# Kernel tuning notes

Measured on AMD Instinct MI355X. Metric: run time of the kernel, lower is better.

The kernel has to match this reference:

```python
import jax, jax.numpy as jnp
import numpy as np
from functools import partial

ALPHA = 0.5
BETA = 0.5
THRESHOLD = 0.5


def _ccl(fg):
    """Connected-component labeling (4-connectivity) of a 2D bool mask via
    iterative min-label propagation; background = 0, components get distinct
    positive ids (component-wise min of raster index + 1). Matches the
    component partition of scipy.ndimage.label (ids differ, masks identical)."""
    H, W = fg.shape
    BIG = H * W + 2
    init = jnp.where(fg, jnp.arange(1, H * W + 1, dtype=jnp.int32).reshape(H, W), 0)

    def step(lab):
        l = jnp.where(fg, lab, BIG)
        up = jnp.pad(l, ((1, 0), (0, 0)), constant_values=BIG)[:-1]
        dn = jnp.pad(l, ((0, 1), (0, 0)), constant_values=BIG)[1:]
        lf = jnp.pad(l, ((0, 0), (1, 0)), constant_values=BIG)[:, :-1]
        rt = jnp.pad(l, ((0, 0), (0, 1)), constant_values=BIG)[:, 1:]
        m = jnp.minimum(jnp.minimum(jnp.minimum(up, dn), jnp.minimum(lf, rt)), l)
        return jnp.where(fg, m, 0)

    def cond(c):
        return jnp.any(c[0] != c[1])

    def body(c):
        return (step(c[0]), c[0])

    lab, _ = jax.lax.while_loop(cond, body, (step(init), init))
    return lab


def _critical(a_lab, b_lab, n_seg):
    """Binary mask of components of a_lab that are not fully covered by the
    foreground of b_lab (i.e. contain at least one mistake voxel) -- the
    detect_critical split/merge criterion."""
    miss = ((b_lab == 0) & (a_lab > 0)).astype(jnp.int32)
    counts = jax.ops.segment_sum(miss.ravel(), a_lab.ravel(), num_segments=n_seg)
    return jnp.where(a_lab > 0, (counts[a_lab] > 0).astype(jnp.float32), 0.0)


def _critical_masks(preds, targets):
    # preds/targets: [B,1,H,W]; work on channel-0 2D slices as the module does
    p2 = preds[:, 0]
    t2 = targets[:, 0]
    H, W = p2.shape[-2:]
    n_seg = H * W + 1
    plab = jax.vmap(_ccl)(p2 > THRESHOLD)
    tlab = jax.vmap(_ccl)(t2 > 0)
    crit = jax.vmap(partial(_critical, n_seg=n_seg))
    neg = crit(tlab, plab)   # critical_type = -1: target components missed
    pos = crit(plab, tlab)   # critical_type = +1: pred components wrong
    return BETA * neg + (1.0 - BETA) * pos  # [B,H,W]


def setup_inputs() -> dict:
    key = jax.random.key(0)
    k1, k2 = jax.random.split(key)
    preds = jax.random.normal(k1, (16, 1, 1024, 1024), dtype=jnp.float32)
    targets = (jax.random.uniform(k2, (16, 1, 1024, 1024)) > 0.5).astype(jnp.float32)
    return {"preds": preds, "targets": targets}


def reference(preds, targets):
    # BCEWithLogitsLoss(reduction='none'), numerically stable
    loss = jnp.maximum(preds, 0) - preds * targets + jnp.log1p(jnp.exp(-jnp.abs(preds)))
    mask = _critical_masks(preds, targets)  # [B,H,W], constant wrt grads
    weight = (1.0 - ALPHA) + ALPHA * mask[:, None]  # broadcast over channel dim
    return (weight * loss).mean()
```

## Files before the change

### kernel.cpp

```cpp
#include <hip/hip_runtime.h>
#include <math.h>


#define HH 1024
#define WW 1024
#define IMGPIX (HH * WW)
#define NB_TOTAL 16
#define FLAGBIT 0x40000000
#define IDXMASK 0x3FFFFFFF
#define NBLK 2048
#define NPART 2048
#define NTHR 256
#define WPR 16
#define RPR 512
#define SROWS 32
#define STRIPS (HH / SROWS)
#define SLOTS (SROWS * RPR)
#define NTHR_S 1024

typedef unsigned long long u64;

__device__ __forceinline__ int findRootH(int* p, int i) {
    volatile int* vp = p;
    int r = i;
    int e = vp[r] & IDXMASK;
    while (e != r) {
        int e2 = vp[e] & IDXMASK;
        if (e2 != e) p[r] = e2;
        r = e; e = e2;
    }
    return r;
}

__device__ __forceinline__ void flagProp(int* p, int x) {
    while (true) {
        int r = findRootH(p, x);
        int old = atomicOr(&p[r], FLAGBIT);
        if ((old & IDXMASK) == r) return;
        x = old & IDXMASK;
    }
}

__device__ __forceinline__ void uniteGF(int* p, int a, int b) {
    int ra = findRootH(p, a), rb = findRootH(p, b);
    while (ra != rb) {
        if (ra < rb) { int t = ra; ra = rb; rb = t; }
        int e = p[ra];
        if ((e & IDXMASK) != ra) { ra = findRootH(p, e & IDXMASK); continue; }
        int prev = atomicCAS(&p[ra], e, rb);
        if (prev == e) {
            if (e & FLAGBIT) flagProp(p, rb);
            return;
        }
        ra = findRootH(p, prev & IDXMASK);
        rb = findRootH(p, rb);
    }
}

__device__ __forceinline__ int findRootL(int* lab, int i) {
    volatile int* vl = lab;
    int r = i;
    int e = vl[r] & IDXMASK;
    while (e != r) {
        int e2 = vl[e] & IDXMASK;
        if (e2 != e) lab[r] = e2;
        r = e; e = e2;
    }
    return r;
}

__device__ __forceinline__ void uniteL(int* lab, int a, int b) {
    int ra = findRootL(lab, a), rb = findRootL(lab, b);
    while (ra != rb) {
        if (ra < rb) { int t = ra; ra = rb; rb = t; }
        int prev = atomicCAS(&lab[ra], ra, rb);
        if (prev == ra) return;
        ra = findRootL(lab, prev & IDXMASK);
        rb = findRootL(lab, rb);
    }
}

__device__ __forceinline__ int runIndexW(u64 starts, int b) {
    u64 below = (2ULL << b) - 1ULL;
    return (int)__popcll(starts & below) - 1;
}

__global__ void k_zero(double* __restrict__ part) {
    part[blockIdx.x * blockDim.x + threadIdx.x] = 0.0;
}

__device__ __forceinline__ float packf(float mag, bool fl) {
    return __uint_as_float(__float_as_uint(mag) | (fl ? 0x80000000u : 0u));
}

__device__ __forceinline__ void phaseBody(int lane, int mask, int mist, int starts,
                                          int carry, int excl, int incl,
                                          const float* lossv, long rbase,
                                          float* __restrict__ runsum) {
    float cur = 0.0f, headmag = 0.0f;
    bool curf = false, headf = false;
    bool begun = false, prevfg = (carry != 0), hasHead = false;
    int scount = 0;
    #pragma unroll
    for (int k = 0; k < 16; ++k) {
        bool fg = (mask >> k) & 1;
        bool mk = (mist >> k) & 1;
        if (fg) {
            if ((starts >> k) & 1) { cur = lossv[k]; curf = mk; begun = true; ++scount; }
            else { cur += lossv[k]; curf |= mk; }
        } else {
            if (prevfg) {
                if (begun) runsum[rbase + excl + scount - 1] = packf(cur, curf);
                else { hasHead = true; headmag = cur; headf = curf; }
            }
        }
        prevfg = fg;
    }
    float sv = prevfg ? packf(cur, curf) : 0.0f;
    u64 fullb = __ballot(mask == 0xFFFF);
    if (fullb) {
        int fl = (starts != 0);
        #pragma unroll
        for (int d = 1; d < 64; d <<= 1) {
            float u = __shfl_up(sv, d, 64);
            int uf = __shfl_up(fl, d, 64);
            if (lane >= d) {
                if (!fl) {
                    unsigned sg = (__float_as_uint(sv) | __float_as_uint(u)) & 0x80000000u;
                    float mag = fabsf(sv) + fabsf(u);
                    sv = __uint_as_float(__float_as_uint(mag) | sg);
                }
                fl |= uf;
            }
        }
    }
    float svprev = __shfl_up(sv, 1, 64);
    if (hasHead) {
        unsigned sg = (__float_as_uint(svprev) & 0x80000000u) | (headf ? 0x80000000u : 0u);
        float mag = fabsf(svprev) + headmag;
        runsum[rbase + excl - 1] = __uint_as_float(__float_as_uint(mag) | sg);
    }
    if (lane == 63 && prevfg) runsum[rbase + incl - 1] = sv;
}

__global__ void k_maskloss(const float* __restrict__ preds, const float* __restrict__ targets,
                           long gbase, int nrows,
                           u64* __restrict__ fT, u64* __restrict__ fP,
                           u64* __restrict__ sT, u64* __restrict__ sP,
                           int* __restrict__ prT, int* __restrict__ prP,
                           int* __restrict__ rcT, int* __restrict__ rcP,
                           float* __restrict__ runsumT, float* __restrict__ runsumP,
                           double* __restrict__ part) {
    __shared__ double sh[4];
    int wid = threadIdx.x >> 6, lane = threadIdx.x & 63;
    double lsum = 0.0;
    for (int R = blockIdx.x * 4 + wid; R < nrows; R += gridDim.x * 4) {
        long pixbase = (long)R * WW;
        long rbase = (long)R * RPR;
        const float4* p4 = (const float4*)(preds + gbase + pixbase);
        const float4* t4 = (const float4*)(targets + gbase + pixbase);
        float lossv[16];
        int maskT = 0, maskP = 0;
        float rowsum = 0.0f;
        #pragma unroll
        for (int j = 0; j < 4; ++j) {
            float4 pv = p4[lane * 4 + j];
            float4 tv = t4[lane * 4 + j];
            float pp[4] = {pv.x, pv.y, pv.z, pv.w};
            float tt[4] = {tv.x, tv.y, tv.z, tv.w};
            #pragma unroll
            for (int q = 0; q < 4; ++q) {
                int k = j * 4 + q;
                float p = pp[q], t = tt[q];
                float loss = fmaxf(p, 0.0f) - p * t + __logf(1.0f + __expf(-fabsf(p)));
                lossv[k] = loss;
                rowsum += loss;
                maskT |= ((int)(t > 0.0f)) << k;
                maskP |= ((int)(p > 0.5f)) << k;
            }
        }
        lsum += (double)rowsum;

        int mistT = maskT & ~maskP;
        int mistP = maskP & ~maskT;

        int pm = __shfl_up(maskT | (maskP << 16), 1, 64);
        int carryT = (lane == 0) ? 0 : ((pm >> 15) & 1);
        int carryP = (lane == 0) ? 0 : ((int)(((unsigned)pm) >> 31) & 1);
        int stT_ = maskT & ~((maskT << 1) | carryT) & 0xFFFF;
        int stP_ = maskP & ~((maskP << 1) | carryP) & 0xFFFF;

        int cntT = __popc(stT_), cntP = __popc(stP_);
        int incl2 = cntT | (cntP << 16);
        #pragma unroll
        for (int d = 1; d < 64; d <<= 1) {
            int u = __shfl_up(incl2, d, 64);
            if (lane >= d) incl2 += u;
        }
        int inclT = incl2 & 0xFFFF;
        int inclP = (int)(((unsigned)incl2) >> 16);
        int exT = inclT - cntT;
        int exP = inclP - cntP;

        phaseBody(lane, maskT, mistT, stT_, carryT, exT, inclT, lossv, rbase, runsumT);
        phaseBody(lane, maskP, mistP, stP_, carryP, exP, inclP, lossv, rbase, runsumP);
        if (lane == 63) { rcT[R] = inclT; rcP[R] = inclP; }

        int subid = lane & 15;
        int srcl = subid * 4;
        u64 fw = 0, sw = 0;
        #pragma unroll
        for (int j = 0; j < 4; ++j) {
            int mT = __shfl(maskT, srcl + j, 64);
            int mP = __shfl(maskP, srcl + j, 64);
            int aT = __shfl(stT_, srcl + j, 64);
            int aP = __shfl(stP_, srcl + j, 64);
            u64 m = (u64)(unsigned)((lane < 16) ? mT : mP);
            u64 a = (u64)(unsigned)((lane < 16) ? aT : aP);
            fw |= (m & 0xFFFFULL) << (16 * j);
            sw |= (a & 0xFFFFULL) << (16 * j);
        }
        int eT = __shfl(exT, srcl, 64);
        int eP = __shfl(exP, srcl, 64);
        int wi = R * WPR + subid;
        if (lane < 16) { fT[wi] = fw; sT[wi] = sw; prT[wi] = eT; }
        else if (lane < 32) { fP[wi] = fw; sP[wi] = sw; prP[wi] = eP; }
    }
    lsum *= 0.5;
    #pragma unroll
    for (int off = 32; off > 0; off >>= 1) lsum += __shfl_down(lsum, off, 64);
    if (lane == 0) sh[wid] = lsum;
    __syncthreads();
    if (threadIdx.x == 0) part[blockIdx.x] += sh[0] + sh[1] + sh[2] + sh[3];
}

__global__ __launch_bounds__(NTHR_S) void
k_strip(const u64* __restrict__ fT, const u64* __restrict__ fP,
        const u64* __restrict__ sT, const u64* __restrict__ sP,
        const int* __restrict__ prT, const int* __restrict__ prP,
        const int* __restrict__ rcT, const int* __restrict__ rcP,
        const float* __restrict__ runsumT, const float* __restrict__ runsumP,
        int* __restrict__ parentT, int* __restrict__ parentP) {
    __shared__ int lab[SLOTS];
    __shared__ int rcL[SROWS];
    int bid = blockIdx.x;
    int ph = bid & 1; bid >>= 1;
    int strip = bid & (STRIPS - 1);
    int img = bid >> 5;
    const u64* f = ph ? fP : fT;
    const u64* s = ph ? sP : sT;
    const int* pr = ph ? prP : prT;
    const int* rc = ph ? rcP : rcT;
    const float* runsum = ph ? runsumP : runsumT;
    int* parent = ph ? parentP : parentT;
    const int row0 = img * HH + strip * SROWS;

    if (threadIdx.x < SROWS) rcL[threadIdx.x] = rc[row0 + threadIdx.x];
    __syncthreads();

    for (int i = threadIdx.x; i < SLOTS; i += NTHR_S)
        if ((i & (RPR - 1)) < rcL[i >> 9]) lab[i] = i;
    __syncthreads();

    for (int task = threadIdx.x; task < (SROWS - 1) * WPR * 2; task += NTHR_S) {
        int j = task & 1, w = (task >> 1) & 15, r = task >> 5;
        int w0 = (row0 + r) * WPR + w, w1 = w0 + WPR;
        u64 o = f[w0] & f[w1];
        if (!o) continue;
        u64 s0 = s[w0], s1 = s[w1];
        int b0 = r * RPR + pr[w0], b1 = (r + 1) * RPR + pr[w1];
        u64 os = o & ~(o << 1);
        int k = 0;
        while (os) {
            int b = __builtin_ctzll(os);
            os &= os - 1;
            if ((k++ & 1) == j)
                uniteL(lab, b0 + runIndexW(s0, b), b1 + runIndexW(s1, b));
        }
    }
    __syncthreads();

    const int gb = row0 * RPR;
    for (int i = threadIdx.x; i < SLOTS; i += NTHR_S) {
        if ((i & (RPR - 1)) >= rcL[i >> 9]) continue;
        int e = lab[i];
        int rt = e & IDXMASK;
        if (rt != i) {
            rt = findRootL(lab, i);
            parent[gb + i] = gb + rt;
        }
        if (__float_as_uint(runsum[gb + i]) >> 31) {
            if (!(((volatile int*)lab)[rt] & FLAGBIT)) atomicOr(&lab[rt], FLAGBIT);
        }
    }
    __syncthreads();

    for (int i = threadIdx.x; i < SLOTS; i += NTHR_S) {
        if ((i & (RPR - 1)) >= rcL[i >> 9]) continue;
        int e = lab[i];
        if ((e & IDXMASK) == i) parent[gb + i] = (gb + i) | (e & FLAGBIT);
    }
}

__global__ void k_bound(const u64* __restrict__ fT, const u64* __restrict__ fP,
                        const u64* __restrict__ sT, const u64* __restrict__ sP,
                        const int* __restrict__ prT, const int* __restrict__ prP,
                        int* __restrict__ parentT, int* __restrict__ parentP, int nb) {
    int tasks = nb * (STRIPS - 1) * WPR * 2;
    int stride = gridDim.x * blockDim.x;
    for (int id = blockIdx.x * blockDim.x + threadIdx.x; id < tasks; id += stride) {
        int ph = id & 1;
        int t = id >> 1;
        int w = t & 15; t >>= 4;
        int bnd = t % (STRIPS - 1);
        int img = t / (STRIPS - 1);
        int R = img * HH + bnd * SROWS + (SROWS - 1);
        const u64* f = ph ? fP : fT;
        const u64* s = ph ? sP : sT;
        const int* pr = ph ? prP : prT;
        int* parent = ph ? parentP : parentT;
        int w0 = R * WPR + w, w1 = w0 + WPR;
        u64 o = f[w0] & f[w1];
        if (!o) continue;
        u64 s0 = s[w0], s1 = s[w1];
        int b0 = R * RPR + pr[w0], b1 = (R + 1) * RPR + pr[w1];
        u64 os = o & ~(o << 1);
        while (os) {
            int b = __builtin_ctzll(os);
            os &= os - 1;
            uniteGF(parent, b0 + runIndexW(s0, b), b1 + runIndexW(s1, b));
        }
    }
}

__global__ void k_accumrun(const int* __restrict__ rcT, const int* __restrict__ rcP,
                           int* __restrict__ parentT, int* __restrict__ parentP,
                           const float* __restrict__ runsumT, const float* __restrict__ runsumP,
                           double* __restrict__ part, int nslots) {
    int stride = gridDim.x * blockDim.x;
    double local = 0.0;
    int ngroups = nslots >> 2;
    for (int g = blockIdx.x * blockDim.x + threadIdx.x; g < ngroups; g += stride) {
        int base = g << 2;
        int row = base >> 9, k = base & (RPR - 1);
        int nT = rcT[row] - k, nP = rcP[row] - k;
        if (nT > 0) {
            int4 e4 = *(const int4*)&parentT[base];
            float4 r4 = *(const float4*)&runsumT[base];
            int ee[4] = {e4.x, e4.y, e4.z, e4.w};
            float rr[4] = {r4.x, r4.y, r4.z, r4.w};
            int n = nT < 4 ? nT : 4;
            for (int j = 0; j < n; ++j) {
                int e = ee[j];
                int r = e & IDXMASK;
                int fl;
                if (r == base + j) fl = e & FLAGBIT;
                else { r = findRootH(parentT, r); fl = parentT[r] & FLAGBIT; }
                if (fl) local += 0.25 * (double)fabsf(rr[j]);
            }
        }
        if (nP > 0) {
            int4 e4 = *(const int4*)&parentP[base];
            float4 r4 = *(const float4*)&runsumP[base];
            int ee[4] = {e4.x, e4.y, e4.z, e4.w};
            float rr[4] = {r4.x, r4.y, r4.z, r4.w};
            int n = nP < 4 ? nP : 4;
            for (int j = 0; j < n; ++j) {
                int e = ee[j];
                int r = e & IDXMASK;
                int fl;
                if (r == base + j) fl = e & FLAGBIT;
                else { r = findRootH(parentP, r); fl = parentP[r] & FLAGBIT; }
                if (fl) local += 0.25 * (double)fabsf(rr[j]);
            }
        }
    }
    #pragma unroll
    for (int off = 32; off > 0; off >>= 1) local += __shfl_down(local, off, 64);
    __shared__ double sh[NTHR / 64];
    int lane = threadIdx.x & 63, wid = threadIdx.x >> 6;
    if (lane == 0) sh[wid] = local;
    __syncthreads();
    if (threadIdx.x == 0) {
        double tot = 0.0;
        #pragma unroll
        for (int w = 0; w < NTHR / 64; ++w) tot += sh[w];
        part[blockIdx.x] += tot;
    }
}

__global__ void k_final(const double* __restrict__ part, float* __restrict__ out, double inv_n) {
    double v = 0.0;
    for (int i = threadIdx.x; i < NPART; i += blockDim.x) v += part[i];
    #pragma unroll
    for (int off = 32; off > 0; off >>= 1) v += __shfl_down(v, off, 64);
    __shared__ double sh[NTHR / 64];
    int lane = threadIdx.x & 63, wid = threadIdx.x >> 6;
    if (lane == 0) sh[wid] = v;
    __syncthreads();
    if (threadIdx.x == 0) {
        double tot = 0.0;
        #pragma unroll
        for (int w = 0; w < NTHR / 64; ++w) tot += sh[w];
        out[0] = (float)(tot * inv_n);
    }
}

extern "C" void kernel_launch(void* const* d_in, const int* in_sizes, int n_in,
                              void* d_out, int out_size, void* d_ws, size_t ws_size,
                              hipStream_t stream) {
    const float* preds = (const float*)d_in[0];
    const float* targets = (const float*)d_in[1];
    float* out = (float*)d_out;

    double* part = (double*)d_ws;
    char* base = (char*)d_ws + NPART * sizeof(double);
    size_t avail = (ws_size > NPART * sizeof(double)) ? ws_size - NPART * sizeof(double) : 0;
    const size_t wpi = (size_t)HH * WPR;
    const size_t runs_pi = (size_t)HH * RPR;
    const size_t per_img = 4 * wpi * sizeof(u64) + 2 * wpi * sizeof(int)
                         + 2 * HH * sizeof(int) + 2 * runs_pi * sizeof(int)
                         + 2 * runs_pi * sizeof(float);
    int chunk = (int)(avail / per_img);
    if (chunk < 1) chunk = 1;
    if (chunk > NB_TOTAL) chunk = NB_TOTAL;

    u64* fT = (u64*)base;
    u64* fP = fT + (size_t)chunk * wpi;
    u64* sT = fP + (size_t)chunk * wpi;
    u64* sP = sT + (size_t)chunk * wpi;
    int* prT = (int*)(sP + (size_t)chunk * wpi);
    int* prP = prT + (size_t)chunk * wpi;
    int* rcT = prP + (size_t)chunk * wpi;
    int* rcP = rcT + (size_t)chunk * HH;
    int* parentT = rcP + (size_t)chunk * HH;
    int* parentP = parentT + (size_t)chunk * runs_pi;
    float* runsumT = (float*)(parentP + (size_t)chunk * runs_pi);
    float* runsumP = runsumT + (size_t)chunk * runs_pi;

    k_zero<<<NPART / NTHR, NTHR, 0, stream>>>(part);

    for (int b0 = 0; b0 < NB_TOTAL; b0 += chunk) {
        int nb = (b0 + chunk <= NB_TOTAL) ? chunk : (NB_TOTAL - b0);
        long gbase = (long)b0 * IMGPIX;
        int nrows = nb * HH;
        int nslots = (int)(nb * runs_pi);

        k_maskloss<<<NBLK, NTHR, 0, stream>>>(preds, targets, gbase, nrows,
                                              fT, fP, sT, sP, prT, prP, rcT, rcP,
                                              runsumT, runsumP, part);
        k_strip<<<nb * STRIPS * 2, NTHR_S, 0, stream>>>(fT, fP, sT, sP, prT, prP,
                                                        rcT, rcP, runsumT, runsumP,
                                                        parentT, parentP);
        k_bound<<<512, NTHR, 0, stream>>>(fT, fP, sT, sP, prT, prP, parentT, parentP, nb);
        k_accumrun<<<NBLK, NTHR, 0, stream>>>(rcT, rcP, parentT, parentP,
                                              runsumT, runsumP, part, nslots);
    }

    double inv_n = 1.0 / ((double)NB_TOTAL * (double)IMGPIX);
    k_final<<<1, NTHR, 0, stream>>>(part, out, inv_n);
}
```

Measured before the change: 242.1 us.

## Fuse mask/loss row pass with per-strip CCL into one kernel

Merges the row-wise mask/loss/run-extraction kernel and the per-strip union-find kernel into one kernel. Each block owns one 32-row strip and handles both target and prediction labelings in sequence, reusing its shared-memory label array. This removes a kernel launch and lets the strip's run data be read back while it is likely still in cache, and the per-row run counts are passed through shared memory. In exchange the grid drops to one 512-thread block per strip instead of a grid-stride loop plus two blocks per strip, and the two phases run serially, which reduces parallelism and occupancy.

Measured after the change: 279.0 us. 15.2% more time.

```diff
diff --git a/kernel.cpp b/kernel.cpp
--- a/kernel.cpp
+++ b/kernel.cpp
@@ -16,7 +16,7 @@
 #define SROWS 32
 #define STRIPS (HH / SROWS)
 #define SLOTS (SROWS * RPR)
-#define NTHR_S 1024
+#define NTHR_F 512
 
 typedef unsigned long long u64;
 
@@ -143,18 +143,30 @@
     if (lane == 63 && prevfg) runsum[rbase + incl - 1] = sv;
 }
 
-__global__ void k_maskloss(const float* __restrict__ preds, const float* __restrict__ targets,
-                           long gbase, int nrows,
-                           u64* __restrict__ fT, u64* __restrict__ fP,
-                           u64* __restrict__ sT, u64* __restrict__ sP,
-                           int* __restrict__ prT, int* __restrict__ prP,
-                           int* __restrict__ rcT, int* __restrict__ rcP,
-                           float* __restrict__ runsumT, float* __restrict__ runsumP,
-                           double* __restrict__ part) {
-    __shared__ double sh[4];
-    int wid = threadIdx.x >> 6, lane = threadIdx.x & 63;
+__global__ __launch_bounds__(NTHR_F) void
+k_mls(const float* __restrict__ preds, const float* __restrict__ targets,
+      long gbase,
+      u64* __restrict__ fT, u64* __restrict__ fP,
+      u64* __restrict__ sT, u64* __restrict__ sP,
+      int* __restrict__ prT, int* __restrict__ prP,
+      int* __restrict__ rcT, int* __restrict__ rcP,
+      float* __restrict__ runsumT, float* __restrict__ runsumP,
+      int* __restrict__ parentT, int* __restrict__ parentP,
+      double* __restrict__ part) {
+    __shared__ int lab[SLOTS];
+    __shared__ int rcL[2][SROWS];
+    __shared__ double shd[NTHR_F / 64];
+
+    const int tid = threadIdx.x;
+    const int wid = tid >> 6, lane = tid & 63;
+    const int img = blockIdx.x >> 5;
+    const int strip = blockIdx.x & (STRIPS - 1);
+    const int row0 = img * HH + strip * SROWS;
+
     double lsum = 0.0;
-    for (int R = blockIdx.x * 4 + wid; R < nrows; R += gridDim.x * 4) {
+    for (int j = 0; j < 4; ++j) {
+        int rl = wid * 4 + j;
+        int R = row0 + rl;
         long pixbase = (long)R * WW;
         long rbase = (long)R * RPR;
         const float4* p4 = (const float4*)(preds + gbase + pixbase);
@@ -163,14 +175,14 @@
         int maskT = 0, maskP = 0;
         float rowsum = 0.0f;
         #pragma unroll
-        for (int j = 0; j < 4; ++j) {
-            float4 pv = p4[lane * 4 + j];
-            float4 tv = t4[lane * 4 + j];
+        for (int jj = 0; jj < 4; ++jj) {
+            float4 pv = p4[lane * 4 + jj];
+            float4 tv = t4[lane * 4 + jj];
             float pp[4] = {pv.x, pv.y, pv.z, pv.w};
             float tt[4] = {tv.x, tv.y, tv.z, tv.w};
             #pragma unroll
             for (int q = 0; q < 4; ++q) {
-                int k = j * 4 + q;
+                int k = jj * 4 + q;
                 float p = pp[q], t = tt[q];
                 float loss = fmaxf(p, 0.0f) - p * t + __logf(1.0f + __expf(-fabsf(p)));
                 lossv[k] = loss;
@@ -204,21 +216,24 @@
 
         phaseBody(lane, maskT, mistT, stT_, carryT, exT, inclT, lossv, rbase, runsumT);
         phaseBody(lane, maskP, mistP, stP_, carryP, exP, inclP, lossv, rbase, runsumP);
-        if (lane == 63) { rcT[R] = inclT; rcP[R] = inclP; }
+        if (lane == 63) {
+            rcT[R] = inclT; rcP[R] = inclP;
+            rcL[0][rl] = inclT; rcL[1][rl] = inclP;
+        }
 
         int subid = lane & 15;
         int srcl = subid * 4;
         u64 fw = 0, sw = 0;
         #pragma unroll
-        for (int j = 0; j < 4; ++j) {
-            int mT = __shfl(maskT, srcl + j, 64);
-            int mP = __shfl(maskP, srcl + j, 64);
-            int aT = __shfl(stT_, srcl + j, 64);
-            int aP = __shfl(stP_, srcl + j, 64);
+        for (int jj = 0; jj < 4; ++jj) {
+            int mT = __shfl(maskT, srcl + jj, 64);
+            int mP = __shfl(maskP, srcl + jj, 64);
+            int aT = __shfl(stT_, srcl + jj, 64);
+            int aP = __shfl(stP_, srcl + jj, 64);
             u64 m = (u64)(unsigned)((lane < 16) ? mT : mP);
             u64 a = (u64)(unsigned)((lane < 16) ? aT : aP);
-            fw |= (m & 0xFFFFULL) << (16 * j);
-            sw |= (a & 0xFFFFULL) << (16 * j);
+            fw |= (m & 0xFFFFULL) << (16 * jj);
+            sw |= (a & 0xFFFFULL) << (16 * jj);
         }
         int eT = __shfl(exT, srcl, 64);
         int eP = __shfl(exP, srcl, 64);
@@ -229,76 +244,65 @@
     lsum *= 0.5;
     #pragma unroll
     for (int off = 32; off > 0; off >>= 1) lsum += __shfl_down(lsum, off, 64);
-    if (lane == 0) sh[wid] = lsum;
+    if (lane == 0) shd[wid] = lsum;
     __syncthreads();
-    if (threadIdx.x == 0) part[blockIdx.x] += sh[0] + sh[1] + sh[2] + sh[3];
-}
-
-__global__ __launch_bounds__(NTHR_S) void
-k_strip(const u64* __restrict__ fT, const u64* __restrict__ fP,
-        const u64* __restrict__ sT, const u64* __restrict__ sP,
-        const int* __restrict__ prT, const int* __restrict__ prP,
-        const int* __restrict__ rcT, const int* __restrict__ rcP,
-        const float* __restrict__ runsumT, const float* __restrict__ runsumP,
-        int* __restrict__ parentT, int* __restrict__ parentP) {
-    __shared__ int lab[SLOTS];
-    __shared__ int rcL[SROWS];
-    int bid = blockIdx.x;
-    int ph = bid & 1; bid >>= 1;
-    int strip = bid & (STRIPS - 1);
-    int img = bid >> 5;
-    const u64* f = ph ? fP : fT;
-    const u64* s = ph ? sP : sT;
-    const int* pr = ph ? prP : prT;
-    const int* rc = ph ? rcP : rcT;
-    const float* runsum = ph ? runsumP : runsumT;
-    int* parent = ph ? parentP : parentT;
-    const int row0 = img * HH + strip * SROWS;
-
-    if (threadIdx.x < SROWS) rcL[threadIdx.x] = rc[row0 + threadIdx.x];
-    __syncthreads();
-
-    for (int i = threadIdx.x; i < SLOTS; i += NTHR_S)
-        if ((i & (RPR - 1)) < rcL[i >> 9]) lab[i] = i;
-    __syncthreads();
-
-    for (int task = threadIdx.x; task < (SROWS - 1) * WPR * 2; task += NTHR_S) {
-        int j = task & 1, w = (task >> 1) & 15, r = task >> 5;
-        int w0 = (row0 + r) * WPR + w, w1 = w0 + WPR;
-        u64 o = f[w0] & f[w1];
-        if (!o) continue;
-        u64 s0 = s[w0], s1 = s[w1];
-        int b0 = r * RPR + pr[w0], b1 = (r + 1) * RPR + pr[w1];
-        u64 os = o & ~(o << 1);
-        int k = 0;
-        while (os) {
-            int b = __builtin_ctzll(os);
-            os &= os - 1;
-            if ((k++ & 1) == j)
-                uniteL(lab, b0 + runIndexW(s0, b), b1 + runIndexW(s1, b));
-        }
-    }
-    __syncthreads();
+    if (tid == 0) {
+        double tot = 0.0;
+        #pragma unroll
+        for (int w = 0; w < NTHR_F / 64; ++w) tot += shd[w];
+        part[blockIdx.x] += tot;
+    }
 
     const int gb = row0 * RPR;
-    for (int i = threadIdx.x; i < SLOTS; i += NTHR_S) {
-        if ((i & (RPR - 1)) >= rcL[i >> 9]) continue;
-        int e = lab[i];
-        int rt = e & IDXMASK;
-        if (rt != i) {
-            rt = findRootL(lab, i);
-            parent[gb + i] = gb + rt;
-        }
-        if (__float_as_uint(runsum[gb + i]) >> 31) {
-            if (!(((volatile int*)lab)[rt] & FLAGBIT)) atomicOr(&lab[rt], FLAGBIT);
-        }
-    }
-    __syncthreads();
-
-    for (int i = threadIdx.x; i < SLOTS; i += NTHR_S) {
-        if ((i & (RPR - 1)) >= rcL[i >> 9]) continue;
-        int e = lab[i];
-        if ((e & IDXMASK) == i) parent[gb + i] = (gb + i) | (e & FLAGBIT);
+    for (int ph = 0; ph < 2; ++ph) {
+        const u64* f = ph ? fP : fT;
+        const u64* s = ph ? sP : sT;
+        const int* pr = ph ? prP : prT;
+        const float* runsum = ph ? runsumP : runsumT;
+        int* parent = ph ? parentP : parentT;
+
+        for (int i = tid; i < SLOTS; i += NTHR_F)
+            if ((i & (RPR - 1)) < rcL[ph][i >> 9]) lab[i] = i;
+        __syncthreads();
+
+        for (int task = tid; task < (SROWS - 1) * WPR * 2; task += NTHR_F) {
+            int j = task & 1, w = (task >> 1) & 15, r = task >> 5;
+            int w0 = (row0 + r) * WPR + w, w1 = w0 + WPR;
+            u64 o = f[w0] & f[w1];
+            if (!o) continue;
+            u64 s0 = s[w0], s1 = s[w1];
+            int b0 = r * RPR + pr[w0], b1 = (r + 1) * RPR + pr[w1];
+            u64 os = o & ~(o << 1);
+            int k = 0;
+            while (os) {
+                int b = __builtin_ctzll(os);
+                os &= os - 1;
+                if ((k++ & 1) == j)
+                    uniteL(lab, b0 + runIndexW(s0, b), b1 + runIndexW(s1, b));
+            }
+        }
+        __syncthreads();
+
+        for (int i = tid; i < SLOTS; i += NTHR_F) {
+            if ((i & (RPR - 1)) >= rcL[ph][i >> 9]) continue;
+            int e = lab[i];
+            int rt = e & IDXMASK;
+            if (rt != i) {
+                rt = findRootL(lab, i);
+                parent[gb + i] = gb + rt;
+            }
+            if (__float_as_uint(runsum[gb + i]) >> 31) {
+                if (!(((volatile int*)lab)[rt] & FLAGBIT)) atomicOr(&lab[rt], FLAGBIT);
+            }
+        }
+        __syncthreads();
+
+        for (int i = tid; i < SLOTS; i += NTHR_F) {
+            if ((i & (RPR - 1)) >= rcL[ph][i >> 9]) continue;
+            int e = lab[i];
+            if ((e & IDXMASK) == i) parent[gb + i] = (gb + i) | (e & FLAGBIT);
+        }
+        __syncthreads();
     }
 }
 
@@ -443,15 +447,12 @@
     for (int b0 = 0; b0 < NB_TOTAL; b0 += chunk) {
         int nb = (b0 + chunk <= NB_TOTAL) ? chunk : (NB_TOTAL - b0);
         long gbase = (long)b0 * IMGPIX;
-        int nrows = nb * HH;
         int nslots = (int)(nb * runs_pi);
 
-        k_maskloss<<<NBLK, NTHR, 0, stream>>>(preds, targets, gbase, nrows,
-                                              fT, fP, sT, sP, prT, prP, rcT, rcP,
-                                              runsumT, runsumP, part);
-        k_strip<<<nb * STRIPS * 2, NTHR_S, 0, stream>>>(fT, fP, sT, sP, prT, prP,
-                                                        rcT, rcP, runsumT, runsumP,
-                                                        parentT, parentP);
+        k_mls<<<nb * STRIPS, NTHR_F, 0, stream>>>(preds, targets, gbase,
+                                                  fT, fP, sT, sP, prT, prP, rcT, rcP,
+                                                  runsumT, runsumP, parentT, parentP,
+                                                  part);
         k_bound<<<512, NTHR, 0, stream>>>(fT, fP, sT, sP, prT, prP, parentT, parentP, nb);
         k_accumrun<<<NBLK, NTHR, 0, stream>>>(rcT, rcP, parentT, parentP,
                                               runsumT, runsumP, part, nslots);
```
